# Optimization experiments

Hardware: AMD Instinct MI355X
Metric: run time of the kernel (lower is better)

The kernel has to match this reference:

```python
import jax, jax.numpy as jnp
import numpy as np

QLEN, MLEN, BSZ, DMODEL, NHEAD, DHEAD, DFF = 1024, 1024, 4, 1024, 16, 64, 4096
KLEN = QLEN + MLEN


def _layernorm(x, g, b, eps=1e-5):
    mu = jnp.mean(x, axis=-1, keepdims=True)
    var = jnp.var(x, axis=-1, keepdims=True)
    return (x - mu) * jax.lax.rsqrt(var + eps) * g + b


def _rel_shift(x):
    # x: [qlen, klen, bsz, nhead] -- Transformer-XL shift trick
    q, k, b, n = x.shape
    x = jnp.pad(x, ((0, 0), (1, 0), (0, 0), (0, 0)))  # [q, k+1, b, n]
    x = x.reshape(k + 1, q, b, n)[1:]
    return x.reshape(q, k, b, n)


def setup_inputs() -> dict:
    key = jax.random.key(0)
    ks = jax.random.split(key, 16)
    s = 0.02
    inp = {
        "word_embed": jax.random.normal(ks[0], (QLEN, BSZ, DMODEL), jnp.float32),
        "pos_embed": jax.random.normal(ks[1], (KLEN, DMODEL), jnp.float32),
        "bias_q": jax.random.normal(ks[2], (NHEAD, DHEAD), jnp.float32) * s,
        "bias_k": jax.random.normal(ks[3], (NHEAD, DHEAD), jnp.float32) * s,
        "memories": jax.random.normal(ks[4], (MLEN, BSZ, DMODEL), jnp.float32),
        "W_qkv": jax.random.normal(ks[5], (DMODEL, 3 * NHEAD * DHEAD), jnp.float32) * s,
        "W_r": jax.random.normal(ks[6], (DMODEL, NHEAD * DHEAD), jnp.float32) * s,
        "W_o": jax.random.normal(ks[7], (NHEAD * DHEAD, DMODEL), jnp.float32) * s,
        "ln1_g": jnp.ones((DMODEL,), jnp.float32),
        "ln1_b": jnp.zeros((DMODEL,), jnp.float32),
        "W_ff1": jax.random.normal(ks[8], (DMODEL, DFF), jnp.float32) * s,
        "b_ff1": jnp.zeros((DFF,), jnp.float32),
        "W_ff2": jax.random.normal(ks[9], (DFF, DMODEL), jnp.float32) * s,
        "b_ff2": jnp.zeros((DMODEL,), jnp.float32),
        "ln2_g": jnp.ones((DMODEL,), jnp.float32),
        "ln2_b": jnp.zeros((DMODEL,), jnp.float32),
    }
    # causal mask with memory: position i may attend to j <= i + MLEN; True = masked
    i = jnp.arange(QLEN)[:, None]
    j = jnp.arange(KLEN)[None, :]
    inp["attention_mask"] = j > (i + MLEN)
    return inp


def reference(word_embed, pos_embed, bias_q, bias_k, attention_mask, memories,
              W_qkv, W_r, W_o, ln1_g, ln1_b, W_ff1, b_ff1, W_ff2, b_ff2, ln2_g, ln2_b):
    scale = 1.0 / np.sqrt(DHEAD)
    cat = jnp.concatenate([memories, word_embed], axis=0)  # [klen, b, d]
    w_heads = cat @ W_qkv  # [klen, b, 3*n*dh]
    q, k, v = jnp.split(w_heads, 3, axis=-1)
    q = q[-QLEN:].reshape(QLEN, BSZ, NHEAD, DHEAD)
    k = k.reshape(KLEN, BSZ, NHEAD, DHEAD)
    v = v.reshape(KLEN, BSZ, NHEAD, DHEAD)
    r = (pos_embed @ W_r).reshape(KLEN, NHEAD, DHEAD)

    AC = jnp.einsum('ibnd,jbnd->ijbn', q + bias_q, k)          # content term
    BD = jnp.einsum('ibnd,jnd->ijbn', q + bias_k, r)           # position term
    BD = _rel_shift(BD)
    score = (AC + BD) * scale
    score = jnp.where(attention_mask[:, :, None, None], -1e30, score)
    prob = jax.nn.softmax(score, axis=1)
    attn_vec = jnp.einsum('ijbn,jbnd->ibnd', prob, v).reshape(QLEN, BSZ, NHEAD * DHEAD)
    attn_out = attn_vec @ W_o
    out = _layernorm(word_embed + attn_out, ln1_g, ln1_b)       # post-LN (pre_lnorm=False)

    core = jax.nn.relu(out @ W_ff1 + b_ff1) @ W_ff2 + b_ff2
    return _layernorm(out + core, ln2_g, ln2_b)
```

## Files before the change

kernel.cpp:

```cpp
#include <hip/hip_runtime.h>


typedef __bf16 bf16x8 __attribute__((ext_vector_type(8)));
typedef float f32x4 __attribute__((ext_vector_type(4)));

#define DEVI __device__ __forceinline__

DEVI unsigned short f2bf(float f) {
  union { float f; unsigned int u; } v;
  v.f = f;
  unsigned int u = v.u;
  u += 0x7fffu + ((u >> 16) & 1u);
  return (unsigned short)(u >> 16);
}

DEVI void load16(const unsigned short* g, unsigned short* l) {
  __builtin_amdgcn_global_load_lds(
      (const __attribute__((address_space(1))) unsigned int*)g,
      (__attribute__((address_space(3))) unsigned int*)l, 16, 0, 0);
}

__global__ __launch_bounds__(256) void cvt_bf16_kernel(const float* __restrict__ in,
                                                       unsigned short* __restrict__ out) {
  const int i = blockIdx.x * 256 + threadIdx.x;
  float4 v = *(const float4*)(in + (size_t)i * 4);
  ushort4 o;
  o.x = f2bf(v.x);
  o.y = f2bf(v.y);
  o.z = f2bf(v.z);
  o.w = f2bf(v.w);
  *(ushort4*)(out + (size_t)i * 4) = o;
}

template <typename T>
__global__ __launch_bounds__(256) void transpose_to_bf16(
    const T* __restrict__ in, unsigned short* __restrict__ out, int R, int C) {
  __shared__ unsigned short t[64][72];
  const int tid = threadIdx.x;
  const size_t zoff = (size_t)blockIdx.z * R * C;
  const int r0 = blockIdx.y * 64, c0 = blockIdx.x * 64;
  const T* inp = in + zoff;
  unsigned short* outp = out + zoff;
#pragma unroll
  for (int it = 0; it < 4; ++it) {
    int f = tid + 256 * it;
    int r = f >> 4;
    int c4 = (f & 15) << 2;
    if constexpr (sizeof(T) == 4) {
      float4 v = *(const float4*)((const float*)inp + (size_t)(r0 + r) * C + c0 + c4);
      t[c4 + 0][r] = f2bf(v.x);
      t[c4 + 1][r] = f2bf(v.y);
      t[c4 + 2][r] = f2bf(v.z);
      t[c4 + 3][r] = f2bf(v.w);
    } else {
      ushort4 v = *(const ushort4*)((const unsigned short*)inp + (size_t)(r0 + r) * C + c0 + c4);
      t[c4 + 0][r] = v.x;
      t[c4 + 1][r] = v.y;
      t[c4 + 2][r] = v.z;
      t[c4 + 3][r] = v.w;
    }
  }
  __syncthreads();
#pragma unroll
  for (int it = 0; it < 4; ++it) {
    int f = tid + 256 * it;
    int cc = f >> 4;
    int r4 = (f & 15) << 2;
    ushort4 o;
    o.x = t[cc][r4 + 0];
    o.y = t[cc][r4 + 1];
    o.z = t[cc][r4 + 2];
    o.w = t[cc][r4 + 3];
    *(ushort4*)(outp + (size_t)(c0 + cc) * R + r0 + r4) = o;
  }
}

struct GemmArgs {
  const unsigned short* A;
  const unsigned short* Bt;
  int row_split;
  int M, N, K;
  const float* p0;
  const float* p1;
  const float* resid;
  float* outF;
  unsigned short* o0;
  unsigned short* o1;
  unsigned short* o2;
  unsigned short* o3;
  int relu;
};

constexpr int BM = 128, BN = 128, BK = 64;

template <int EPI>
__global__ __launch_bounds__(256, 4) void gemm_kernel(GemmArgs ga) {
  __shared__ __align__(16) unsigned short As[BM * BK];
  __shared__ __align__(16) unsigned short Bs[BN * BK];

  const int n0 = blockIdx.x * BN;
  const int m0 = blockIdx.y * BM;
  if constexpr (EPI == 0) {
    if (n0 + BN <= 1024 && m0 + BM <= ga.row_split) return;
  }
  const int tid = threadIdx.x;
  const int lane = tid & 63;
  const int wv = tid >> 6;
  const int l15 = lane & 15;
  const int quad = lane >> 4;
  const int wm = wv & 1, wn = wv >> 1;
  const int K = ga.K;
  const int r8 = lane >> 3;
  const int sc = (lane & 7) ^ r8;

  const f32x4 fzero = {0.f, 0.f, 0.f, 0.f};
  f32x4 acc[4][4];
#pragma unroll
  for (int i = 0; i < 4; ++i)
#pragma unroll
    for (int j = 0; j < 4; ++j) acc[i][j] = fzero;

  const unsigned short* Ab = ga.A + (size_t)(m0 + 32 * wv + r8) * K + sc * 8;
  const unsigned short* Bb = ga.Bt + (size_t)(n0 + 32 * wv + r8) * K + sc * 8;
  const int h7 = l15 & 7;

  for (int k0 = 0; k0 < K; k0 += BK) {
    __syncthreads();
#pragma unroll
    for (int it = 0; it < 4; ++it)
      load16(Ab + (size_t)(8 * it) * K + k0, &As[(32 * wv + 8 * it) * 64]);
#pragma unroll
    for (int it = 0; it < 4; ++it)
      load16(Bb + (size_t)(8 * it) * K + k0, &Bs[(32 * wv + 8 * it) * 64]);
    __syncthreads();
#pragma unroll
    for (int ks = 0; ks < 2; ++ks) {
      bf16x8 af[4], bg[4];
#pragma unroll
      for (int mt = 0; mt < 4; ++mt)
        af[mt] = *(const bf16x8*)&As[(wm * 64 + mt * 16 + l15) * 64 +
                                     (((ks * 4 + quad) ^ h7) * 8)];
#pragma unroll
      for (int nt = 0; nt < 4; ++nt)
        bg[nt] = *(const bf16x8*)&Bs[(wn * 64 + nt * 16 + l15) * 64 +
                                     (((ks * 4 + quad) ^ h7) * 8)];
#pragma unroll
      for (int mt = 0; mt < 4; ++mt)
#pragma unroll
        for (int nt = 0; nt < 4; ++nt)
          acc[mt][nt] =
              __builtin_amdgcn_mfma_f32_16x16x32_bf16(af[mt], bg[nt], acc[mt][nt], 0, 0, 0);
    }
  }

#pragma unroll
  for (int mt = 0; mt < 4; ++mt) {
#pragma unroll
    for (int nt = 0; nt < 4; ++nt) {
#pragma unroll
      for (int r = 0; r < 4; ++r) {
        const int row = m0 + wm * 64 + mt * 16 + quad * 4 + r;
        const int col = n0 + wn * 64 + nt * 16 + l15;
        float val = acc[mt][nt][r];
        if constexpr (EPI == 0) {
          const int seq = row >> 2, b = row & 3;
          if (col < 1024) {
            if (seq >= 1024) {
              const int nh = col >> 6, d = col & 63;
              const size_t o = ((size_t)((b * 16 + nh) * 1024 + (seq - 1024))) * 64 + d;
              ga.o0[o] = f2bf(val + ga.p0[col]);
              ga.o1[o] = f2bf(val + ga.p1[col]);
            }
          } else if (col < 2048) {
            const int c = col - 1024, nh = c >> 6, d = c & 63, bn = b * 16 + nh;
            const size_t o = (size_t)bn * 131072 +
                             (size_t)(((seq >> 4) * 2 + (d >> 5)) * 512) +
                             ((((d >> 3) & 3) * 16 + (seq & 15)) * 8) + (d & 7);
            ga.o2[o] = f2bf(val);
          } else {
            const int c = col - 2048, nh = c >> 6, d = c & 63, bn = b * 16 + nh;
            const size_t o = (size_t)bn * 131072 + (size_t)((seq >> 7) * 8192) +
                             ((((seq >> 5) & 3) * 4 + (d >> 4)) * 512) +
                             ((((seq >> 3) & 3) * 16 + (d & 15)) * 8) + (seq & 7);
            ga.o3[o] = f2bf(val);
          }
        } else if constexpr (EPI == 1) {
          const int nh = col >> 6, d = col & 63, t = row;
          const size_t o = (size_t)nh * 131072 +
                           (size_t)(((t >> 4) * 2 + (d >> 5)) * 512) +
                           ((((d >> 3) & 3) * 16 + (t & 15)) * 8) + (d & 7);
          ga.o0[o] = f2bf(val);
        } else {
          if (ga.p0) val += ga.p0[col];
          if (ga.resid) val += ga.resid[(size_t)row * ga.N + col];
          if (ga.relu) val = fmaxf(val, 0.f);
          if (ga.outF) ga.outF[(size_t)row * ga.N + col] = val;
          if (ga.o0) ga.o0[(size_t)row * ga.N + col] = f2bf(val);
        }
      }
    }
  }
}

constexpr int P_LD = 136;
constexpr float CEXP = 0.18033688f;

__global__ __launch_bounds__(256, 4) void attn_kernel(
    const unsigned short* __restrict__ QQ, const unsigned short* __restrict__ QK,
    const unsigned short* __restrict__ Kf, const unsigned short* __restrict__ Vf,
    const unsigned short* __restrict__ Rf, unsigned short* __restrict__ AVb) {
  __shared__ __align__(16) unsigned short p_s[4][16 * P_LD];

  const int tid = threadIdx.x;
  const int lane = tid & 63;
  const int wv = tid >> 6;
  const int l15 = lane & 15;
  const int quad = lane >> 4;
  const int bn = blockIdx.x;
  const int y = blockIdx.y;
  const int sel = (wv + y) & 3;
  const int itl = (sel == 0) ? y : (sel == 1) ? 63 - y : (sel == 2) ? 32 + y : 31 - y;
  const int iw = itl * 16;
  const int nh = bn & 15;
  const int bb = bn >> 4;
  unsigned short* pw = &p_s[wv][0];

  const unsigned short* kf = Kf + (size_t)bn * 131072;
  const unsigned short* vf = Vf + (size_t)bn * 131072;
  const unsigned short* rf = Rf + (size_t)nh * 131072;

  const size_t qoff = (size_t)bn * (1024 * 64) + (size_t)(iw + l15) * 64;
  const bf16x8 qq0 = *(const bf16x8*)(QQ + qoff + quad * 8);
  const bf16x8 qq1 = *(const bf16x8*)(QQ + qoff + 32 + quad * 8);
  const bf16x8 qk0 = *(const bf16x8*)(QK + qoff + quad * 8);
  const bf16x8 qk1 = *(const bf16x8*)(QK + qoff + 32 + quad * 8);

  const f32x4 fzero = {0.f, 0.f, 0.f, 0.f};
  f32x4 o_acc[4];
#pragma unroll
  for (int i = 0; i < 4; ++i) o_acc[i] = fzero;
  float lsum[4] = {0.f, 0.f, 0.f, 0.f};

  const int lane8 = lane * 8;
  const int jmax = iw + 15 + 1024;
  for (int j0 = 0; j0 <= jmax; j0 += 128) {
    const int t16b = (j0 >> 4) + 63 - (iw >> 4);
    f32x4 bd[9];
#pragma unroll
    for (int ct = 0; ct < 9; ++ct) {
      int tg = t16b + ct;
      tg = (tg < 127) ? tg : 127;
      const unsigned short* rb = rf + (size_t)(tg * 1024) + lane8;
      bf16x8 b0 = *(const bf16x8*)rb;
      bf16x8 b1 = *(const bf16x8*)(rb + 512);
      f32x4 c = fzero;
      c = __builtin_amdgcn_mfma_f32_16x16x32_bf16(qk0, b0, c, 0, 0, 0);
      c = __builtin_amdgcn_mfma_f32_16x16x32_bf16(qk1, b1, c, 0, 0, 0);
      bd[ct] = c;
    }

    const int ntb = j0 >> 4;
    f32x4 sv[8];
#pragma unroll
    for (int nt = 0; nt < 8; ++nt) {
      const unsigned short* kb = kf + (size_t)((ntb + nt) * 1024) + lane8;
      bf16x8 b0 = *(const bf16x8*)kb;
      bf16x8 b1 = *(const bf16x8*)(kb + 512);
      f32x4 c = fzero;
      c = __builtin_amdgcn_mfma_f32_16x16x32_bf16(qq0, b0, c, 0, 0, 0);
      c = __builtin_amdgcn_mfma_f32_16x16x32_bf16(qq1, b1, c, 0, 0, 0);
      sv[nt] = c;
    }

#pragma unroll
    for (int r = 0; r < 4; ++r) {
      const int il = quad * 4 + r;
      const int u = l15 + 15 - il;
      const int srcl = (lane & 48) | (u & 15);
      float w[9];
#pragma unroll
      for (int ct = 0; ct < 9; ++ct) w[ct] = __shfl(bd[ct][r], srcl, 64);
      const int ig = iw + il;
#pragma unroll
      for (int nt = 0; nt < 8; ++nt) {
        const float bdv = (u & 16) ? w[nt + 1] : w[nt];
        const int jg = j0 + nt * 16 + l15;
        float p = exp2f((sv[nt][r] + bdv) * CEXP);
        p = (jg > ig + 1024) ? 0.f : p;
        lsum[r] += p;
        pw[il * P_LD + nt * 16 + l15] = f2bf(p);
      }
    }

    const unsigned short* vb = vf + (size_t)((j0 >> 7) * 8192) + lane8;
#pragma unroll
    for (int ks = 0; ks < 4; ++ks) {
      bf16x8 ap = *(const bf16x8*)&pw[l15 * P_LD + ks * 32 + quad * 8];
#pragma unroll
      for (int nto = 0; nto < 4; ++nto) {
        bf16x8 bv = *(const bf16x8*)(vb + (ks * 4 + nto) * 512);
        o_acc[nto] = __builtin_amdgcn_mfma_f32_16x16x32_bf16(ap, bv, o_acc[nto], 0, 0, 0);
      }
    }
  }

  float linv[4];
#pragma unroll
  for (int r = 0; r < 4; ++r) {
    float l = lsum[r];
    l += __shfl_xor(l, 1, 64);
    l += __shfl_xor(l, 2, 64);
    l += __shfl_xor(l, 4, 64);
    l += __shfl_xor(l, 8, 64);
    linv[r] = 1.f / l;
  }
#pragma unroll
  for (int nto = 0; nto < 4; ++nto) {
#pragma unroll
    for (int r = 0; r < 4; ++r) {
      const int ig = iw + quad * 4 + r;
      const int d = nto * 16 + l15;
      const float val = o_acc[nto][r] * linv[r];
      AVb[(size_t)(ig * 4 + bb) * 1024 + nh * 64 + d] = f2bf(val);
    }
  }
}

__global__ __launch_bounds__(256) void ln_kernel(const float* __restrict__ x,
                                                 const float* __restrict__ g,
                                                 const float* __restrict__ bta,
                                                 float* __restrict__ outF,
                                                 unsigned short* __restrict__ outB) {
  const int row = blockIdx.x;
  const int tid = threadIdx.x;
  const float* xr = x + (size_t)row * 1024;
  const float4 v = *(const float4*)(xr + tid * 4);
  float s = v.x + v.y + v.z + v.w;
  float ss = v.x * v.x + v.y * v.y + v.z * v.z + v.w * v.w;
#pragma unroll
  for (int off = 1; off < 64; off <<= 1) {
    s += __shfl_xor(s, off, 64);
    ss += __shfl_xor(ss, off, 64);
  }
  __shared__ float red[8];
  const int wv = tid >> 6;
  if ((tid & 63) == 0) {
    red[wv] = s;
    red[4 + wv] = ss;
  }
  __syncthreads();
  s = red[0] + red[1] + red[2] + red[3];
  ss = red[4] + red[5] + red[6] + red[7];
  const float mu = s * (1.f / 1024.f);
  const float var = ss * (1.f / 1024.f) - mu * mu;
  const float rs = rsqrtf(var + 1e-5f);
  const float vv[4] = {v.x, v.y, v.z, v.w};
#pragma unroll
  for (int u = 0; u < 4; ++u) {
    const int c = tid * 4 + u;
    const float y = (vv[u] - mu) * rs * g[c] + bta[c];
    if (outF) outF[(size_t)row * 1024 + c] = y;
    if (outB) outB[(size_t)row * 1024 + c] = f2bf(y);
  }
}

extern "C" void kernel_launch(void* const* d_in, const int* in_sizes, int n_in,
                              void* d_out, int out_size, void* d_ws, size_t ws_size,
                              hipStream_t stream) {
  (void)in_sizes; (void)n_in; (void)out_size; (void)ws_size;
  const float* word_embed = (const float*)d_in[0];
  const float* pos_embed = (const float*)d_in[1];
  const float* bias_q = (const float*)d_in[2];
  const float* bias_k = (const float*)d_in[3];
  const float* memories = (const float*)d_in[4];
  const float* W_qkv = (const float*)d_in[5];
  const float* W_r = (const float*)d_in[6];
  const float* W_o = (const float*)d_in[7];
  const float* ln1_g = (const float*)d_in[8];
  const float* ln1_b = (const float*)d_in[9];
  const float* W_ff1 = (const float*)d_in[10];
  const float* b_ff1 = (const float*)d_in[11];
  const float* W_ff2 = (const float*)d_in[12];
  const float* b_ff2 = (const float*)d_in[13];
  const float* ln2_g = (const float*)d_in[14];
  const float* ln2_b = (const float*)d_in[15];
  float* out = (float*)d_out;

  char* ws = (char*)d_ws;
  unsigned short* QQ = (unsigned short*)(ws + 0);
  unsigned short* QK = (unsigned short*)(ws + 8388608);
  unsigned short* Kf = (unsigned short*)(ws + 16777216);
  unsigned short* Vf = (unsigned short*)(ws + 50331648);
  unsigned short* Rf = (unsigned short*)(ws + 67108864);
  unsigned short* AVb = (unsigned short*)(ws + 71303168);
  float* X1 = (float*)(ws + 79691776);
  float* OUT1 = (float*)(ws + 96468992);
  unsigned short* OUT1b = (unsigned short*)(ws + 113246208);
  unsigned short* Wqkv_t = (unsigned short*)(ws + 121634816);
  unsigned short* Wr_t = (unsigned short*)(ws + 127926272);
  unsigned short* Wo_t = (unsigned short*)(ws + 130023424);
  unsigned short* Wff1_t = (unsigned short*)(ws + 132120576);
  unsigned short* Wff2_t = (unsigned short*)(ws + 140509184);
  unsigned short* Catb = (unsigned short*)(ws + 79691776);
  unsigned short* Posb = (unsigned short*)(ws + 96468992);
  unsigned short* H = (unsigned short*)(ws + 0);
  float* C2 = X1;

  const dim3 blk(256);

  cvt_bf16_kernel<<<4096, blk, 0, stream>>>(memories, Catb);
  cvt_bf16_kernel<<<4096, blk, 0, stream>>>(word_embed, Catb + (size_t)4096 * 1024);
  cvt_bf16_kernel<<<2048, blk, 0, stream>>>(pos_embed, Posb);

  transpose_to_bf16<float><<<dim3(48, 16, 1), blk, 0, stream>>>(W_qkv, Wqkv_t, 1024, 3072);
  transpose_to_bf16<float><<<dim3(16, 16, 1), blk, 0, stream>>>(W_r, Wr_t, 1024, 1024);
  transpose_to_bf16<float><<<dim3(16, 16, 1), blk, 0, stream>>>(W_o, Wo_t, 1024, 1024);
  transpose_to_bf16<float><<<dim3(64, 16, 1), blk, 0, stream>>>(W_ff1, Wff1_t, 1024, 4096);
  transpose_to_bf16<float><<<dim3(16, 64, 1), blk, 0, stream>>>(W_ff2, Wff2_t, 4096, 1024);

  {
    GemmArgs a{};
    a.A = Catb;
    a.row_split = 4096;
    a.Bt = Wqkv_t;
    a.M = 8192; a.N = 3072; a.K = 1024;
    a.p0 = bias_q; a.p1 = bias_k;
    a.o0 = QQ; a.o1 = QK; a.o2 = Kf; a.o3 = Vf;
    gemm_kernel<0><<<dim3(24, 64), blk, 0, stream>>>(a);
  }
  {
    GemmArgs a{};
    a.A = Posb;
    a.Bt = Wr_t;
    a.M = 2048; a.N = 1024; a.K = 1024;
    a.o0 = Rf;
    gemm_kernel<1><<<dim3(8, 16), blk, 0, stream>>>(a);
  }

  attn_kernel<<<dim3(64, 16), blk, 0, stream>>>(QQ, QK, Kf, Vf, Rf, AVb);

  {
    GemmArgs a{};
    a.A = AVb;
    a.Bt = Wo_t;
    a.M = 4096; a.N = 1024; a.K = 1024;
    a.resid = word_embed;
    a.outF = X1;
    gemm_kernel<2><<<dim3(8, 32), blk, 0, stream>>>(a);
  }
  ln_kernel<<<4096, blk, 0, stream>>>(X1, ln1_g, ln1_b, OUT1, OUT1b);

  {
    GemmArgs a{};
    a.A = OUT1b;
    a.Bt = Wff1_t;
    a.M = 4096; a.N = 4096; a.K = 1024;
    a.p0 = b_ff1;
    a.relu = 1;
    a.o0 = H;
    gemm_kernel<2><<<dim3(32, 32), blk, 0, stream>>>(a);
  }
  {
    GemmArgs a{};
    a.A = H;
    a.Bt = Wff2_t;
    a.M = 4096; a.N = 1024; a.K = 4096;
    a.p0 = b_ff2;
    a.resid = OUT1;
    a.outF = C2;
    gemm_kernel<2><<<dim3(8, 32), blk, 0, stream>>>(a);
  }
  ln_kernel<<<4096, blk, 0, stream>>>(C2, ln2_g, ln2_b, out, nullptr);
}
```

Baseline: 675.7 us.

## Split attention key range across wave pairs and combine partials via LDS

```diff
diff --git a/kernel.cpp b/kernel.cpp
--- a/kernel.cpp
+++ b/kernel.cpp
@@ -205,7 +205,7 @@
 constexpr int P_LD = 136;
 constexpr float CEXP = 0.18033688f;
 
-__global__ __launch_bounds__(256, 4) void attn_kernel(
+__global__ __launch_bounds__(256, 8) void attn_kernel(
     const unsigned short* __restrict__ QQ, const unsigned short* __restrict__ QK,
     const unsigned short* __restrict__ Kf, const unsigned short* __restrict__ Vf,
     const unsigned short* __restrict__ Rf, unsigned short* __restrict__ AVb) {
@@ -218,9 +218,9 @@
   const int quad = lane >> 4;
   const int bn = blockIdx.x;
   const int y = blockIdx.y;
-  const int sel = (wv + y) & 3;
-  const int itl = (sel == 0) ? y : (sel == 1) ? 63 - y : (sel == 2) ? 32 + y : 31 - y;
+  const int itl = (wv < 2) ? y : 63 - y;
   const int iw = itl * 16;
+  const int ph = wv & 1;
   const int nh = bn & 15;
   const int bb = bn >> 4;
   unsigned short* pw = &p_s[wv][0];
@@ -243,7 +243,7 @@
 
   const int lane8 = lane * 8;
   const int jmax = iw + 15 + 1024;
-  for (int j0 = 0; j0 <= jmax; j0 += 128) {
+  for (int j0 = ph * 128; j0 <= jmax; j0 += 256) {
     const int t16b = (j0 >> 4) + 63 - (iw >> 4);
     f32x4 bd[9];
 #pragma unroll
@@ -304,7 +304,7 @@
     }
   }
 
-  float linv[4];
+  float lred[4];
 #pragma unroll
   for (int r = 0; r < 4; ++r) {
     float l = lsum[r];
@@ -312,16 +312,38 @@
     l += __shfl_xor(l, 2, 64);
     l += __shfl_xor(l, 4, 64);
     l += __shfl_xor(l, 8, 64);
-    linv[r] = 1.f / l;
-  }
-#pragma unroll
-  for (int nto = 0; nto < 4; ++nto) {
-#pragma unroll
-    for (int r = 0; r < 4; ++r) {
-      const int ig = iw + quad * 4 + r;
-      const int d = nto * 16 + l15;
-      const float val = o_acc[nto][r] * linv[r];
-      AVb[(size_t)(ig * 4 + bb) * 1024 + nh * 64 + d] = f2bf(val);
+    lred[r] = l;
+  }
+
+  float* fb = (float*)&p_s[wv][0];
+  if (ph) {
+#pragma unroll
+    for (int nto = 0; nto < 4; ++nto)
+#pragma unroll
+      for (int r = 0; r < 4; ++r)
+        fb[(quad * 4 + r) * 67 + nto * 16 + l15] = o_acc[nto][r];
+    if (l15 == 0) {
+#pragma unroll
+      for (int r = 0; r < 4; ++r) fb[1072 + quad * 4 + r] = lred[r];
+    }
+  }
+  __syncthreads();
+  if (!ph) {
+    const float* fp = (const float*)&p_s[wv + 1][0];
+    float linv[4];
+#pragma unroll
+    for (int r = 0; r < 4; ++r)
+      linv[r] = 1.f / (lred[r] + fp[1072 + quad * 4 + r]);
+#pragma unroll
+    for (int nto = 0; nto < 4; ++nto) {
+#pragma unroll
+      for (int r = 0; r < 4; ++r) {
+        const int ig = iw + quad * 4 + r;
+        const int d = nto * 16 + l15;
+        const float val =
+            (o_acc[nto][r] + fp[(quad * 4 + r) * 67 + nto * 16 + l15]) * linv[r];
+        AVb[(size_t)(ig * 4 + bb) * 1024 + nh * 64 + d] = f2bf(val);
+      }
     }
   }
 }
@@ -437,7 +459,7 @@
     gemm_kernel<1><<<dim3(8, 16), blk, 0, stream>>>(a);
   }
 
-  attn_kernel<<<dim3(64, 16), blk, 0, stream>>>(QQ, QK, Kf, Vf, Rf, AVb);
+  attn_kernel<<<dim3(64, 32), blk, 0, stream>>>(QQ, QK, Kf, Vf, Rf, AVb);
 
   {
     GemmArgs a{};
```

Result: slower. 989.6 us (+46.5%).
